# Performance work log

Measured on AMD Instinct MI355X. Metric: run time of the kernel, lower is better.

Reference implementation:

```python
import jax, jax.numpy as jnp
import numpy as np

N, H, W, C, K = 8, 512, 512, 3, 5
PAD = K // 2  # odd square kernel, 'same' zero padding


def setup_inputs() -> dict:
    key = jax.random.key(0)
    k1, k2 = jax.random.split(key)
    input_data = jax.random.normal(k1, (N, H, W, C), dtype=jnp.float32)
    # per-sample, per-pixel unshared kernels: (N, H, W, K*K)
    weights = jax.random.normal(k2, (N, H, W, K * K), dtype=jnp.float32) * 0.1
    return {"input_data": input_data, "weights": weights}


def reference(input_data, weights):
    # Local (untied) depthwise conv: out[n,h,w,c] =
    #   sum_{dh,dw} in[n, h+dh-P, w+dw-P, c] * weights[n, h, w, dh*K+dw]
    # Weight is shared across channels (no channel dim in weights).
    x = jnp.pad(input_data, ((0, 0), (PAD, PAD), (PAD, PAD), (0, 0)))
    out = jnp.zeros_like(input_data)
    for k in range(K * K):  # fixed small loop over kernel taps
        dh, dw = k // K, k % K
        out = out + x[:, dh:dh + H, dw:dw + W, :] * weights[..., k:k + 1]
    return out
```

## Files before the change

kernel.cpp:

```cpp
#include <hip/hip_runtime.h>

#define NN 8
#define HH 512
#define WW 512
#define CC 3
#define KK 5
#define PADP 2
#define WROWF (WW * CC)
#define NT 4
#define NBLOCKS (NN * HH * WW / 64 / NT)

typedef float f4a __attribute__((ext_vector_type(4), aligned(4)));

struct Row { f4a L0, L1, L2, L3; };

__device__ __forceinline__ void load_row(const float* rb, Row& r) {
    r.L0 = *(const f4a*)(rb);
    r.L1 = *(const f4a*)(rb + 4);
    r.L2 = *(const f4a*)(rb + 8);
    r.L3 = *(const f4a*)(rb + 11);
}

__device__ __forceinline__ void fma_row(const Row& r, const float* wp,
                                        float& a0, float& a1, float& a2) {
    const float w0 = wp[0], w1 = wp[1], w2 = wp[2], w3 = wp[3], w4 = wp[4];
    a0 = fmaf(r.L0[0], w0, a0); a1 = fmaf(r.L0[1], w0, a1); a2 = fmaf(r.L0[2], w0, a2);
    a0 = fmaf(r.L0[3], w1, a0); a1 = fmaf(r.L1[0], w1, a1); a2 = fmaf(r.L1[1], w1, a2);
    a0 = fmaf(r.L1[2], w2, a0); a1 = fmaf(r.L1[3], w2, a1); a2 = fmaf(r.L2[0], w2, a2);
    a0 = fmaf(r.L2[1], w3, a0); a1 = fmaf(r.L2[2], w3, a1); a2 = fmaf(r.L2[3], w3, a2);
    a0 = fmaf(r.L3[1], w4, a0); a1 = fmaf(r.L3[2], w4, a1); a2 = fmaf(r.L3[3], w4, a2);
}

#define GLDS16(gp, lp) __builtin_amdgcn_global_load_lds( \
    (const __attribute__((address_space(1))) void*)(gp), \
    (__attribute__((address_space(3))) void*)(lp), 16, 0, 0)
#define GLDS4(gp, lp) __builtin_amdgcn_global_load_lds( \
    (const __attribute__((address_space(1))) void*)(gp), \
    (__attribute__((address_space(3))) void*)(lp), 4, 0, 0)

#define STAGE(dst, row) do {                                            \
    const char* _s = (const char*)(wt + ((long)(nHH + (row)) * WW + w0) * (KK * KK)); \
    _Pragma("unroll")                                                   \
    for (int _it = 0; _it < 6; ++_it)                                   \
        GLDS16(_s + _it * 1024 + lane * 16, (dst) + _it * 256);         \
    GLDS4(_s + 6144 + lane * 4, (dst) + 1536);                          \
} while (0)

#define WAITK(N) do {                                                   \
    asm volatile("s_waitcnt vmcnt(" #N ")" ::: "memory");               \
    __builtin_amdgcn_sched_barrier(0);                                  \
} while (0)

#define CTILE(Ra, Rb, Rc, Rd, Re, WBUF, row) do {                       \
    const float* _wp = &WBUF[lane * (KK * KK)];                         \
    float a0 = 0.f, a1 = 0.f, a2 = 0.f;                                 \
    fma_row(Ra, _wp + 0,  a0, a1, a2);                                  \
    fma_row(Rb, _wp + 5,  a0, a1, a2);                                  \
    fma_row(Rc, _wp + 10, a0, a1, a2);                                  \
    fma_row(Rd, _wp + 15, a0, a1, a2);                                  \
    fma_row(Re, _wp + 20, a0, a1, a2);                                  \
    float* _o = out + ((long)(nHH + (row)) * WW + w0 + lane) * CC;      \
    _o[0] = a0; _o[1] = a1; _o[2] = a2;                                 \
} while (0)

#define STILE(WBUF, row) do {                                           \
    const float* _wp = &WBUF[lane * (KK * KK)];                         \
    const int _w = w0 + lane;                                           \
    float a0 = 0.f, a1 = 0.f, a2 = 0.f;                                 \
    _Pragma("unroll")                                                   \
    for (int dh = 0; dh < KK; ++dh) {                                   \
        const int ih = (row) + dh - PADP;                               \
        const bool rok = ((unsigned)ih < (unsigned)HH);                 \
        _Pragma("unroll")                                               \
        for (int dw = 0; dw < KK; ++dw) {                               \
            const int iw = _w + dw - PADP;                              \
            const bool ok = rok && ((unsigned)iw < (unsigned)WW);       \
            const float* p = inb + ((long)(ih * WW + iw)) * CC;         \
            float v0 = ok ? p[0] : 0.f;                                 \
            float v1 = ok ? p[1] : 0.f;                                 \
            float v2 = ok ? p[2] : 0.f;                                 \
            const float wv = _wp[dh * KK + dw];                         \
            a0 = fmaf(v0, wv, a0);                                      \
            a1 = fmaf(v1, wv, a1);                                      \
            a2 = fmaf(v2, wv, a2);                                      \
        }                                                               \
    }                                                                   \
    float* _o = out + ((long)(nHH + (row)) * WW + w0 + lane) * CC;      \
    _o[0] = a0; _o[1] = a1; _o[2] = a2;                                 \
} while (0)

__global__ __launch_bounds__(64, 3) void conv_local_kernel(
    const float* __restrict__ in,
    const float* __restrict__ wt,
    float* __restrict__ out)
{
    __shared__ float bufA[64 * KK * KK];
    __shared__ float bufB[64 * KK * KK];

    const int lane = threadIdx.x;
    const int b    = ((blockIdx.x & 7) << 10) | (blockIdx.x >> 3);
    const int wseg = b & 7;
    const int hg   = (b >> 3) & 127;
    const int n    = b >> 10;
    const int w0   = wseg << 6;
    const int h0   = hg << 2;
    const int nHH  = n * HH;

    const float* inb = in + (size_t)n * (HH * WW * CC);

    STAGE(bufA, h0 + 0);

    const bool interior = (wseg >= 1) && (wseg <= 6) && (hg >= 1) && (hg <= 126);

    if (interior) {
        const float* rb = inb + ((long)(h0 - PADP) * WW + (w0 + lane - PADP)) * CC;
        Row R0, R1, R2, R3, R4, R5, R6, R7;
        load_row(rb + 0 * WROWF, R0);
        load_row(rb + 1 * WROWF, R1);
        load_row(rb + 2 * WROWF, R2);
        load_row(rb + 3 * WROWF, R3);
        load_row(rb + 4 * WROWF, R4);
        STAGE(bufB, h0 + 1);
        load_row(rb + 5 * WROWF, R5);
        WAITK(11);
        CTILE(R0, R1, R2, R3, R4, bufA, h0 + 0);
        STAGE(bufA, h0 + 2);
        load_row(rb + 6 * WROWF, R6);
        WAITK(11);
        CTILE(R1, R2, R3, R4, R5, bufB, h0 + 1);
        STAGE(bufB, h0 + 3);
        load_row(rb + 7 * WROWF, R7);
        WAITK(11);
        CTILE(R2, R3, R4, R5, R6, bufA, h0 + 2);
        WAITK(0);
        CTILE(R3, R4, R5, R6, R7, bufB, h0 + 3);
    } else {
        STAGE(bufB, h0 + 1);
        WAITK(7);
        STILE(bufA, h0 + 0);
        STAGE(bufA, h0 + 2);
        WAITK(7);
        STILE(bufB, h0 + 1);
        STAGE(bufB, h0 + 3);
        WAITK(7);
        STILE(bufA, h0 + 2);
        WAITK(0);
        STILE(bufB, h0 + 3);
    }
}

extern "C" void kernel_launch(void* const* d_in, const int* in_sizes, int n_in,
                              void* d_out, int out_size, void* d_ws, size_t ws_size,
                              hipStream_t stream) {
    const float* in = (const float*)d_in[0];
    const float* wt = (const float*)d_in[1];
    float* out = (float*)d_out;

    conv_local_kernel<<<NBLOCKS, 64, 0, stream>>>(in, wt, out);
}
```

Before: 64.48 us.

## Process 16 rows per block with double-buffered input windows and weight staging

Each block now covers 16 output rows instead of 4, cutting the grid from 8192 to 2048 blocks. The interior path no longer keeps a sliding window of input rows in registers. Instead it reloads a full 5-row window for the next output row into a second register set and overlaps that load with the current row's FMAs and the weight staging into LDS. This amortizes block launch and prologue cost and deepens the prefetch pipeline, but each input row is now read five times instead of about two. It also doubles register use, so occupancy is lowered via launch_bounds(64,2) and fewer blocks are resident.

```diff
diff --git a/kernel.cpp b/kernel.cpp
--- a/kernel.cpp
+++ b/kernel.cpp
@@ -7,12 +7,13 @@
 #define KK 5
 #define PADP 2
 #define WROWF (WW * CC)
-#define NT 4
-#define NBLOCKS (NN * HH * WW / 64 / NT)
+#define NTILES 16
+#define NBLOCKS 2048
 
 typedef float f4a __attribute__((ext_vector_type(4), aligned(4)));
 
 struct Row { f4a L0, L1, L2, L3; };
+struct Win { Row r0, r1, r2, r3, r4; };
 
 __device__ __forceinline__ void load_row(const float* rb, Row& r) {
     r.L0 = *(const f4a*)(rb);
@@ -51,20 +52,36 @@
     __builtin_amdgcn_sched_barrier(0);                                  \
 } while (0)
 
-#define CTILE(Ra, Rb, Rc, Rd, Re, WBUF, row) do {                       \
-    const float* _wp = &WBUF[lane * (KK * KK)];                         \
+#define LOADWIN(W, row) do {                                            \
+    const float* _rb = inb + (long)((row) - PADP) * WROWF + colbase;    \
+    load_row(_rb + 0 * WROWF, (W).r0);                                  \
+    load_row(_rb + 1 * WROWF, (W).r1);                                  \
+    load_row(_rb + 2 * WROWF, (W).r2);                                  \
+    load_row(_rb + 3 * WROWF, (W).r3);                                  \
+    load_row(_rb + 4 * WROWF, (W).r4);                                  \
+} while (0)
+
+#define CTILE(W, WBUF, row) do {                                        \
+    const float* _wp = &(WBUF)[lane * (KK * KK)];                       \
     float a0 = 0.f, a1 = 0.f, a2 = 0.f;                                 \
-    fma_row(Ra, _wp + 0,  a0, a1, a2);                                  \
-    fma_row(Rb, _wp + 5,  a0, a1, a2);                                  \
-    fma_row(Rc, _wp + 10, a0, a1, a2);                                  \
-    fma_row(Rd, _wp + 15, a0, a1, a2);                                  \
-    fma_row(Re, _wp + 20, a0, a1, a2);                                  \
+    fma_row((W).r0, _wp + 0,  a0, a1, a2);                              \
+    fma_row((W).r1, _wp + 5,  a0, a1, a2);                              \
+    fma_row((W).r2, _wp + 10, a0, a1, a2);                              \
+    fma_row((W).r3, _wp + 15, a0, a1, a2);                              \
+    fma_row((W).r4, _wp + 20, a0, a1, a2);                              \
     float* _o = out + ((long)(nHH + (row)) * WW + w0 + lane) * CC;      \
     _o[0] = a0; _o[1] = a1; _o[2] = a2;                                 \
 } while (0)
 
+#define IBODY(CURBUF, NXTBUF, CURW, NXTW, t) do {                       \
+    STAGE(NXTBUF, h0 + (t) + 1);                                        \
+    LOADWIN(NXTW, h0 + (t) + 1);                                        \
+    WAITK(27);                                                          \
+    CTILE(CURW, CURBUF, h0 + (t));                                      \
+} while (0)
+
 #define STILE(WBUF, row) do {                                           \
-    const float* _wp = &WBUF[lane * (KK * KK)];                         \
+    const float* _wp = &(WBUF)[lane * (KK * KK)];                       \
     const int _w = w0 + lane;                                           \
     float a0 = 0.f, a1 = 0.f, a2 = 0.f;                                 \
     _Pragma("unroll")                                                   \
@@ -89,7 +106,13 @@
     _o[0] = a0; _o[1] = a1; _o[2] = a2;                                 \
 } while (0)
 
-__global__ __launch_bounds__(64, 3) void conv_local_kernel(
+#define SBODY(CURBUF, NXTBUF, t) do {                                   \
+    STAGE(NXTBUF, h0 + (t) + 1);                                        \
+    WAITK(7);                                                           \
+    STILE(CURBUF, h0 + (t));                                            \
+} while (0)
+
+__global__ __launch_bounds__(64, 2) void conv_local_kernel(
     const float* __restrict__ in,
     const float* __restrict__ wt,
     float* __restrict__ out)
@@ -98,54 +121,60 @@
     __shared__ float bufB[64 * KK * KK];
 
     const int lane = threadIdx.x;
-    const int b    = ((blockIdx.x & 7) << 10) | (blockIdx.x >> 3);
-    const int wseg = b & 7;
-    const int hg   = (b >> 3) & 127;
-    const int n    = b >> 10;
+    const int b    = ((blockIdx.x & 7) << 8) | (blockIdx.x >> 3);
+    const int n    = b >> 8;
+    const int rem  = b & 255;
+    const int wseg = rem & 7;
+    const int seg  = rem >> 3;
     const int w0   = wseg << 6;
-    const int h0   = hg << 2;
+    const int h0   = seg << 4;
     const int nHH  = n * HH;
 
     const float* inb = in + (size_t)n * (HH * WW * CC);
+    const int colbase = (w0 + lane - PADP) * CC;
 
-    STAGE(bufA, h0 + 0);
+    const bool interior = (wseg >= 1) && (wseg <= 6) && (seg >= 1) && (seg <= 30);
 
-    const bool interior = (wseg >= 1) && (wseg <= 6) && (hg >= 1) && (hg <= 126);
+    STAGE(bufA, h0);
 
     if (interior) {
-        const float* rb = inb + ((long)(h0 - PADP) * WW + (w0 + lane - PADP)) * CC;
-        Row R0, R1, R2, R3, R4, R5, R6, R7;
-        load_row(rb + 0 * WROWF, R0);
-        load_row(rb + 1 * WROWF, R1);
-        load_row(rb + 2 * WROWF, R2);
-        load_row(rb + 3 * WROWF, R3);
-        load_row(rb + 4 * WROWF, R4);
-        STAGE(bufB, h0 + 1);
-        load_row(rb + 5 * WROWF, R5);
-        WAITK(11);
-        CTILE(R0, R1, R2, R3, R4, bufA, h0 + 0);
-        STAGE(bufA, h0 + 2);
-        load_row(rb + 6 * WROWF, R6);
-        WAITK(11);
-        CTILE(R1, R2, R3, R4, R5, bufB, h0 + 1);
-        STAGE(bufB, h0 + 3);
-        load_row(rb + 7 * WROWF, R7);
-        WAITK(11);
-        CTILE(R2, R3, R4, R5, R6, bufA, h0 + 2);
+        Win WA, WB;
+        LOADWIN(WA, h0);
+        IBODY(bufA, bufB, WA, WB, 0);
+        IBODY(bufB, bufA, WB, WA, 1);
+        IBODY(bufA, bufB, WA, WB, 2);
+        IBODY(bufB, bufA, WB, WA, 3);
+        IBODY(bufA, bufB, WA, WB, 4);
+        IBODY(bufB, bufA, WB, WA, 5);
+        IBODY(bufA, bufB, WA, WB, 6);
+        IBODY(bufB, bufA, WB, WA, 7);
+        IBODY(bufA, bufB, WA, WB, 8);
+        IBODY(bufB, bufA, WB, WA, 9);
+        IBODY(bufA, bufB, WA, WB, 10);
+        IBODY(bufB, bufA, WB, WA, 11);
+        IBODY(bufA, bufB, WA, WB, 12);
+        IBODY(bufB, bufA, WB, WA, 13);
+        IBODY(bufA, bufB, WA, WB, 14);
         WAITK(0);
-        CTILE(R3, R4, R5, R6, R7, bufB, h0 + 3);
+        CTILE(WB, bufB, h0 + 15);
     } else {
-        STAGE(bufB, h0 + 1);
-        WAITK(7);
-        STILE(bufA, h0 + 0);
-        STAGE(bufA, h0 + 2);
-        WAITK(7);
-        STILE(bufB, h0 + 1);
-        STAGE(bufB, h0 + 3);
-        WAITK(7);
-        STILE(bufA, h0 + 2);
+        SBODY(bufA, bufB, 0);
+        SBODY(bufB, bufA, 1);
+        SBODY(bufA, bufB, 2);
+        SBODY(bufB, bufA, 3);
+        SBODY(bufA, bufB, 4);
+        SBODY(bufB, bufA, 5);
+        SBODY(bufA, bufB, 6);
+        SBODY(bufB, bufA, 7);
+        SBODY(bufA, bufB, 8);
+        SBODY(bufB, bufA, 9);
+        SBODY(bufA, bufB, 10);
+        SBODY(bufB, bufA, 11);
+        SBODY(bufA, bufB, 12);
+        SBODY(bufB, bufA, 13);
+        SBODY(bufA, bufB, 14);
         WAITK(0);
-        STILE(bufB, h0 + 3);
+        STILE(bufB, h0 + 15);
     }
 }
 
```

New measurement: 85.77 us. +33.0%, slower.

## Remap blocks to full output rows with looped double-buffered weight staging

Applied to the files above, without the earlier changes.

Each block now covers one full image row, walking 8 column segments in a loop, instead of a 4-row by 64-column tile. Weight staging into LDS stays double-buffered. The fast vector path now covers every row away from the top and bottom borders. Column-edge lanes fall back to a per-lane guarded scalar recompute, with input addresses clamped so the vector loads stay in bounds. The goal is to widen the fast path and simplify the schedule, but the block now reloads 5 input rows per output row instead of reusing a sliding window of rows across 4 output rows.

```diff
diff --git a/kernel.cpp b/kernel.cpp
--- a/kernel.cpp
+++ b/kernel.cpp
@@ -7,8 +7,7 @@
 #define KK 5
 #define PADP 2
 #define WROWF (WW * CC)
-#define NT 4
-#define NBLOCKS (NN * HH * WW / 64 / NT)
+#define NBLOCKS 4096
 
 typedef float f4a __attribute__((ext_vector_type(4), aligned(4)));
 
@@ -38,12 +37,12 @@
     (const __attribute__((address_space(1))) void*)(gp), \
     (__attribute__((address_space(3))) void*)(lp), 4, 0, 0)
 
-#define STAGE(dst, row) do {                                            \
-    const char* _s = (const char*)(wt + ((long)(nHH + (row)) * WW + w0) * (KK * KK)); \
+#define STAGE(dst, jj) do {                                             \
+    const char* _s = (const char*)(wt + (rowbase + ((long)(jj) << 6)) * (KK * KK)); \
     _Pragma("unroll")                                                   \
     for (int _it = 0; _it < 6; ++_it)                                   \
         GLDS16(_s + _it * 1024 + lane * 16, (dst) + _it * 256);         \
-    GLDS4(_s + 6144 + lane * 4, (dst) + 1536);                          \
+    GLDS4(_s + 6144 + lane * 4, (dst) + 1536);                         \
 } while (0)
 
 #define WAITK(N) do {                                                   \
@@ -51,31 +50,63 @@
     __builtin_amdgcn_sched_barrier(0);                                  \
 } while (0)
 
-#define CTILE(Ra, Rb, Rc, Rd, Re, WBUF, row) do {                       \
-    const float* _wp = &WBUF[lane * (KK * KK)];                         \
+#define LOADIN(jj) do {                                                 \
+    int _wc = ((jj) << 6) + lane - PADP;                                \
+    _wc = _wc < 0 ? 0 : (_wc > 507 ? 507 : _wc);                        \
+    const float* _rb = inb + (long)(h - PADP) * WROWF + _wc * CC;       \
+    load_row(_rb + 0 * WROWF, R0);                                      \
+    load_row(_rb + 1 * WROWF, R1);                                      \
+    load_row(_rb + 2 * WROWF, R2);                                      \
+    load_row(_rb + 3 * WROWF, R3);                                      \
+    load_row(_rb + 4 * WROWF, R4);                                      \
+} while (0)
+
+#define COMPUTE(BUF, jj) do {                                           \
+    const float* _wp = &(BUF)[lane * (KK * KK)];                        \
     float a0 = 0.f, a1 = 0.f, a2 = 0.f;                                 \
-    fma_row(Ra, _wp + 0,  a0, a1, a2);                                  \
-    fma_row(Rb, _wp + 5,  a0, a1, a2);                                  \
-    fma_row(Rc, _wp + 10, a0, a1, a2);                                  \
-    fma_row(Rd, _wp + 15, a0, a1, a2);                                  \
-    fma_row(Re, _wp + 20, a0, a1, a2);                                  \
-    float* _o = out + ((long)(nHH + (row)) * WW + w0 + lane) * CC;      \
+    fma_row(R0, _wp + 0,  a0, a1, a2);                                  \
+    fma_row(R1, _wp + 5,  a0, a1, a2);                                  \
+    fma_row(R2, _wp + 10, a0, a1, a2);                                  \
+    fma_row(R3, _wp + 15, a0, a1, a2);                                  \
+    fma_row(R4, _wp + 20, a0, a1, a2);                                  \
+    const int _w = ((jj) << 6) + lane;                                  \
+    if (_w < PADP || _w >= WW - PADP) {      \
+        a0 = 0.f; a1 = 0.f; a2 = 0.f;                                   \
+        _Pragma("unroll")                                               \
+        for (int dh = 0; dh < KK; ++dh) {                               \
+            const int ih = h + dh - PADP;                               \
+            _Pragma("unroll")                                           \
+            for (int dw = 0; dw < KK; ++dw) {                           \
+                const int iw = _w + dw - PADP;                          \
+                const bool ok = ((unsigned)iw < (unsigned)WW);          \
+                const float* p = inb + ((long)ih * WW + iw) * CC;       \
+                float v0 = ok ? p[0] : 0.f;                             \
+                float v1 = ok ? p[1] : 0.f;                             \
+                float v2 = ok ? p[2] : 0.f;                             \
+                const float wv = _wp[dh * KK + dw];                     \
+                a0 = fmaf(v0, wv, a0);                                  \
+                a1 = fmaf(v1, wv, a1);                                  \
+                a2 = fmaf(v2, wv, a2);                                  \
+            }                                                           \
+        }                                                               \
+    }                                                                   \
+    float* _o = out + (rowbase + _w) * CC;                              \
     _o[0] = a0; _o[1] = a1; _o[2] = a2;                                 \
 } while (0)
 
-#define STILE(WBUF, row) do {                                           \
-    const float* _wp = &WBUF[lane * (KK * KK)];                         \
-    const int _w = w0 + lane;                                           \
+#define SCALAR(BUF, jj) do {                                            \
+    const float* _wp = &(BUF)[lane * (KK * KK)];                        \
+    const int _w = ((jj) << 6) + lane;                                  \
     float a0 = 0.f, a1 = 0.f, a2 = 0.f;                                 \
     _Pragma("unroll")                                                   \
     for (int dh = 0; dh < KK; ++dh) {                                   \
-        const int ih = (row) + dh - PADP;                               \
+        const int ih = h + dh - PADP;                                   \
         const bool rok = ((unsigned)ih < (unsigned)HH);                 \
         _Pragma("unroll")                                               \
         for (int dw = 0; dw < KK; ++dw) {                               \
             const int iw = _w + dw - PADP;                              \
             const bool ok = rok && ((unsigned)iw < (unsigned)WW);       \
-            const float* p = inb + ((long)(ih * WW + iw)) * CC;         \
+            const float* p = inb + ((long)ih * WW + iw) * CC;           \
             float v0 = ok ? p[0] : 0.f;                                 \
             float v1 = ok ? p[1] : 0.f;                                 \
             float v2 = ok ? p[2] : 0.f;                                 \
@@ -85,7 +116,7 @@
             a2 = fmaf(v2, wv, a2);                                      \
         }                                                               \
     }                                                                   \
-    float* _o = out + ((long)(nHH + (row)) * WW + w0 + lane) * CC;      \
+    float* _o = out + (rowbase + _w) * CC;                              \
     _o[0] = a0; _o[1] = a1; _o[2] = a2;                                 \
 } while (0)
 
@@ -98,54 +129,42 @@
     __shared__ float bufB[64 * KK * KK];
 
     const int lane = threadIdx.x;
-    const int b    = ((blockIdx.x & 7) << 10) | (blockIdx.x >> 3);
-    const int wseg = b & 7;
-    const int hg   = (b >> 3) & 127;
-    const int n    = b >> 10;
-    const int w0   = wseg << 6;
-    const int h0   = hg << 2;
-    const int nHH  = n * HH;
+    const int b = ((blockIdx.x & 7) << 9) | (blockIdx.x >> 3);
+    const int n = b >> 9;
+    const int h = b & (HH - 1);
+    const long rowbase = (long)(n * HH + h) * WW;
 
     const float* inb = in + (size_t)n * (HH * WW * CC);
+    const bool rowok = (h >= PADP) && (h < HH - PADP);
 
-    STAGE(bufA, h0 + 0);
+    float* cur = bufA;
+    float* nxt = bufB;
 
-    const bool interior = (wseg >= 1) && (wseg <= 6) && (hg >= 1) && (hg <= 126);
+    STAGE(cur, 0);
 
-    if (interior) {
-        const float* rb = inb + ((long)(h0 - PADP) * WW + (w0 + lane - PADP)) * CC;
-        Row R0, R1, R2, R3, R4, R5, R6, R7;
-        load_row(rb + 0 * WROWF, R0);
-        load_row(rb + 1 * WROWF, R1);
-        load_row(rb + 2 * WROWF, R2);
-        load_row(rb + 3 * WROWF, R3);
-        load_row(rb + 4 * WROWF, R4);
-        STAGE(bufB, h0 + 1);
-        load_row(rb + 5 * WROWF, R5);
-        WAITK(11);
-        CTILE(R0, R1, R2, R3, R4, bufA, h0 + 0);
-        STAGE(bufA, h0 + 2);
-        load_row(rb + 6 * WROWF, R6);
-        WAITK(11);
-        CTILE(R1, R2, R3, R4, R5, bufB, h0 + 1);
-        STAGE(bufB, h0 + 3);
-        load_row(rb + 7 * WROWF, R7);
-        WAITK(11);
-        CTILE(R2, R3, R4, R5, R6, bufA, h0 + 2);
+    if (rowok) {
+        Row R0, R1, R2, R3, R4;
+        LOADIN(0);
+#pragma unroll 1
+        for (int j = 0; j < 7; ++j) {
+            STAGE(nxt, j + 1);
+            WAITK(7);
+            COMPUTE(cur, j);
+            LOADIN(j + 1);
+            float* t = cur; cur = nxt; nxt = t;
+        }
         WAITK(0);
-        CTILE(R3, R4, R5, R6, R7, bufB, h0 + 3);
+        COMPUTE(cur, 7);
     } else {
-        STAGE(bufB, h0 + 1);
-        WAITK(7);
-        STILE(bufA, h0 + 0);
-        STAGE(bufA, h0 + 2);
-        WAITK(7);
-        STILE(bufB, h0 + 1);
-        STAGE(bufB, h0 + 3);
-        WAITK(7);
-        STILE(bufA, h0 + 2);
+#pragma unroll 1
+        for (int j = 0; j < 7; ++j) {
+            STAGE(nxt, j + 1);
+            WAITK(7);
+            SCALAR(cur, j);
+            float* t = cur; cur = nxt; nxt = t;
+        }
         WAITK(0);
-        STILE(bufB, h0 + 3);
+        SCALAR(cur, 7);
     }
 }
 
```

New measurement: 130.1 us. 2.02x slower.
